# Kernel optimization log

Hardware: AMD Instinct MI355X
Metric: run time of the kernel (lower is better)

Reference implementation:

```python
import jax, jax.numpy as jnp
import numpy as np
import math

L = 2          # num_layers
H = 1024       # hidden_dim
NH = 16        # num_heads
HD = H // NH   # head_dim = 64
M = 4096       # mlp_dim
GRIDS = [(2, 32, 32), (1, 32, 32)]  # (t,h,w) per image -> 2048 + 1024 = 3072 tokens
THETA = 10000.0
EPS = 1e-5


def _rope_cos_sin(grids, head_dim):
    # Rope2DPosEmbRepeated: interleaved (x,y) complex rotations, repeated over t.
    n = head_dim // 4
    freqs = 1.0 / (THETA ** (np.arange(0, head_dim, 4, dtype=np.float64)[:n] / head_dim))
    parts = []
    for t, h, w in grids:
        ys, xs = np.meshgrid(np.arange(h), np.arange(w), indexing='ij')
        xa = xs.reshape(-1, 1).astype(np.float64) * freqs  # [h*w, n]
        ya = ys.reshape(-1, 1).astype(np.float64) * freqs
        ang = np.stack([xa, ya], axis=-1).reshape(-1, head_dim // 2)  # interleave x,y
        parts.append(np.tile(ang, (t, 1)))
    ang = np.concatenate(parts, axis=0).astype(np.float32)  # [S, head_dim//2]
    return jnp.asarray(np.cos(ang)), jnp.asarray(np.sin(ang))


def _segment_ids(grids):
    lens = [t * h * w for t, h, w in grids]
    return jnp.asarray(np.repeat(np.arange(len(lens)), lens))


def _layernorm(x, g, b):
    mu = jnp.mean(x, axis=-1, keepdims=True)
    var = jnp.mean(jnp.square(x - mu), axis=-1, keepdims=True)
    return (x - mu) * jax.lax.rsqrt(var + EPS) * g + b


def _apply_rope(x, cos, sin):
    # x: [S, NH, HD]; cos/sin: [S, HD//2] -> broadcast over heads (unsqueeze(-2))
    xr = x.reshape(x.shape[0], x.shape[1], HD // 2, 2)
    a, b = xr[..., 0], xr[..., 1]
    c = cos[:, None, :]
    s = sin[:, None, :]
    oa = a * c - b * s
    ob = a * s + b * c
    return jnp.stack([oa, ob], axis=-1).reshape(x.shape)


def setup_inputs() -> dict:
    key = jax.random.key(0)
    ks = jax.random.split(key, 8)
    S = sum(t * h * w for t, h, w in GRIDS)
    sH = 1.0 / math.sqrt(H)
    sM = 1.0 / math.sqrt(M)
    return {
        'hidden_states': jax.random.normal(ks[0], (S, H), jnp.float32),
        'grid_thws': jnp.asarray(np.array(GRIDS, dtype=np.int32)),
        'ln0_g': jnp.ones((L, H), jnp.float32),
        'ln0_b': jnp.zeros((L, H), jnp.float32),
        'wqkv': jax.random.normal(ks[1], (L, 3 * H, H), jnp.float32) * sH,
        'wo': jax.random.normal(ks[2], (L, H, H), jnp.float32) * sH,
        'ln1_g': jnp.ones((L, H), jnp.float32),
        'ln1_b': jnp.zeros((L, H), jnp.float32),
        'fc0_w': jax.random.normal(ks[3], (L, M, H), jnp.float32) * math.sqrt(2.0 / H),
        'fc0_b': jnp.zeros((L, M), jnp.float32),
        'fc1_w': jax.random.normal(ks[4], (L, H, M), jnp.float32) * math.sqrt(2.0 / M),
        'fc1_b': jnp.zeros((L, H), jnp.float32),
        'fln_g': jnp.ones((H,), jnp.float32),
        'fln_b': jnp.zeros((H,), jnp.float32),
    }


def reference(hidden_states, grid_thws, ln0_g, ln0_b, wqkv, wo, ln1_g, ln1_b,
              fc0_w, fc0_b, fc1_w, fc1_b, fln_g, fln_b):
    grids = [tuple(int(v) for v in row) for row in np.asarray(grid_thws)]
    S = hidden_states.shape[0]
    cos, sin = _rope_cos_sin(grids, HD)
    seg = _segment_ids(grids)
    mask = seg[:, None] == seg[None, :]  # block-diagonal [S, S]
    scale = 1.0 / math.sqrt(HD)

    x = hidden_states
    for i in range(L):
        h = _layernorm(x, ln0_g[i], ln0_b[i])
        qkv = (h @ wqkv[i].T).reshape(S, 3, NH, HD)
        q, k, v = qkv[:, 0], qkv[:, 1], qkv[:, 2]
        q = _apply_rope(q, cos, sin)
        k = _apply_rope(k, cos, sin)
        scores = jnp.einsum('qhd,khd->hqk', q, k) * scale
        scores = jnp.where(mask[None], scores, -1e30)
        attn = jax.nn.softmax(scores, axis=-1)
        o = jnp.einsum('hqk,khd->qhd', attn, v).reshape(S, H)
        x = x + o @ wo[i].T
        h2 = _layernorm(x, ln1_g[i], ln1_b[i])
        mlp = jax.nn.gelu(h2 @ fc0_w[i].T + fc0_b[i], approximate=False) @ fc1_w[i].T + fc1_b[i]
        x = x + mlp
    return _layernorm(x, fln_g, fln_b)
```

## Files before the change

kernel.cpp:

```cpp
#include <hip/hip_runtime.h>
#include <hip/hip_bf16.h>
#include <cstdint>
#include <math.h>

constexpr int ST   = 3072;
constexpr int HH   = 1024;
constexpr int NHD  = 16;
constexpr int DH   = 64;
constexpr int MMLP = 4096;
constexpr int SEG0 = 2048;

using short8 = __attribute__((ext_vector_type(8))) short;
using f32x4  = __attribute__((ext_vector_type(4))) float;

#if __has_builtin(__builtin_amdgcn_exp2f)
#define EXP2F __builtin_amdgcn_exp2f
#else
#define EXP2F exp2f
#endif

#if __has_builtin(__builtin_amdgcn_rcpf)
#define RCPF __builtin_amdgcn_rcpf
#else
#define RCPF(x) (1.f / (x))
#endif

__device__ __forceinline__ unsigned short f2bf(float f) {
  unsigned int u = __float_as_uint(f);
  u += 0x7fffu + ((u >> 16) & 1u);
  return (unsigned short)(u >> 16);
}

__device__ __forceinline__ float bf2f_lo(unsigned int u) {
  return __uint_as_float(u << 16);
}
__device__ __forceinline__ float bf2f_hi(unsigned int u) {
  return __uint_as_float(u & 0xffff0000u);
}

__device__ __forceinline__ void g2l16(const void* g, void* l) {
  __builtin_amdgcn_global_load_lds(
      (const __attribute__((address_space(1))) unsigned int*)g,
      (__attribute__((address_space(3))) unsigned int*)l, 16, 0, 0);
}

__device__ __forceinline__ float erf_fast(float z) {
  const float az = fabsf(z);
  const float t1 = RCPF(1.f + 0.3275911f * az);
  const float poly =
      t1 * (0.254829592f +
            t1 * (-0.284496736f +
                  t1 * (1.421413741f +
                        t1 * (-1.453152027f + t1 * 1.061405429f))));
  const float e = EXP2F(-az * az * 1.4426950408889634f);
  const float v = 1.f - poly * e;
  return (z < 0.f) ? -v : v;
}

__global__ void cast_all(const float* __restrict__ s0,
                         const float* __restrict__ s1,
                         const float* __restrict__ s2,
                         const float* __restrict__ s3,
                         ushort4* __restrict__ dst) {
  const int i = blockIdx.x * blockDim.x + threadIdx.x;
  const float4* src;
  int off;
  if (i < 1572864)      { src = (const float4*)s0; off = i; }
  else if (i < 2097152) { src = (const float4*)s1; off = i - 1572864; }
  else if (i < 4194304) { src = (const float4*)s2; off = i - 2097152; }
  else                  { src = (const float4*)s3; off = i - 4194304; }
  const float4 v = src[off];
  ushort4 u;
  u.x = f2bf(v.x); u.y = f2bf(v.y); u.z = f2bf(v.z); u.w = f2bf(v.w);
  dst[i] = u;
}

__global__ void ln_kernel(const float* __restrict__ x,
                          const float* __restrict__ g,
                          const float* __restrict__ b,
                          unsigned short* obf) {
  const int s = blockIdx.x;
  const int t = threadIdx.x;
  const float4 v = ((const float4*)(x + (size_t)s * HH))[t];
  float s1 = v.x + v.y + v.z + v.w;
  float s2 = v.x * v.x + v.y * v.y + v.z * v.z + v.w * v.w;
#pragma unroll
  for (int off = 32; off > 0; off >>= 1) {
    s1 += __shfl_down(s1, off);
    s2 += __shfl_down(s2, off);
  }
  __shared__ float red[8];
  __shared__ float stat[2];
  const int wv = t >> 6, ln = t & 63;
  if (ln == 0) { red[wv] = s1; red[4 + wv] = s2; }
  __syncthreads();
  if (t == 0) {
    float a1 = red[0] + red[1] + red[2] + red[3];
    float a2 = red[4] + red[5] + red[6] + red[7];
    float mu = a1 * (1.f / HH);
    float var = a2 * (1.f / HH) - mu * mu;
    stat[0] = mu;
    stat[1] = rsqrtf(var + 1e-5f);
  }
  __syncthreads();
  const float mu = stat[0], rs = stat[1];
  const float4 gg = ((const float4*)g)[t];
  const float4 bb = ((const float4*)b)[t];
  ushort4 u;
  u.x = f2bf((v.x - mu) * rs * gg.x + bb.x);
  u.y = f2bf((v.y - mu) * rs * gg.y + bb.y);
  u.z = f2bf((v.z - mu) * rs * gg.z + bb.z);
  u.w = f2bf((v.w - mu) * rs * gg.w + bb.w);
  ((ushort4*)(obf + (size_t)s * HH))[t] = u;
}

template <int NS>
__global__ void ln_comb(const float* __restrict__ xin,
                        const unsigned short* __restrict__ Pb,
                        const float* __restrict__ bias,
                        const float* __restrict__ g,
                        const float* __restrict__ b,
                        float* __restrict__ xout,
                        unsigned short* obf, float* of) {
  const int s = blockIdx.x;
  const int t = threadIdx.x;
  const size_t row = (size_t)s * HH;
  const size_t sl = (size_t)ST * HH;
  float4 v = ((const float4*)(xin + row))[t];
#pragma unroll
  for (int c = 0; c < NS; ++c) {
    const uint2 p = ((const uint2*)(Pb + c * sl + row))[t];
    v.x += bf2f_lo(p.x); v.y += bf2f_hi(p.x);
    v.z += bf2f_lo(p.y); v.w += bf2f_hi(p.y);
  }
  if (bias) {
    const float4 bb4 = ((const float4*)bias)[t];
    v.x += bb4.x; v.y += bb4.y; v.z += bb4.z; v.w += bb4.w;
  }
  if (xout) ((float4*)(xout + row))[t] = v;
  float s1 = v.x + v.y + v.z + v.w;
  float s2 = v.x * v.x + v.y * v.y + v.z * v.z + v.w * v.w;
#pragma unroll
  for (int off = 32; off > 0; off >>= 1) {
    s1 += __shfl_down(s1, off);
    s2 += __shfl_down(s2, off);
  }
  __shared__ float red[8];
  __shared__ float stat[2];
  const int wv = t >> 6, ln = t & 63;
  if (ln == 0) { red[wv] = s1; red[4 + wv] = s2; }
  __syncthreads();
  if (t == 0) {
    float a1 = red[0] + red[1] + red[2] + red[3];
    float a2 = red[4] + red[5] + red[6] + red[7];
    float mu = a1 * (1.f / HH);
    float var = a2 * (1.f / HH) - mu * mu;
    stat[0] = mu;
    stat[1] = rsqrtf(var + 1e-5f);
  }
  __syncthreads();
  const float mu = stat[0], rs = stat[1];
  const float4 gg = ((const float4*)g)[t];
  const float4 bb = ((const float4*)b)[t];
  float4 o;
  o.x = (v.x - mu) * rs * gg.x + bb.x;
  o.y = (v.y - mu) * rs * gg.y + bb.y;
  o.z = (v.z - mu) * rs * gg.z + bb.z;
  o.w = (v.w - mu) * rs * gg.w + bb.w;
  if (obf) {
    ushort4 u;
    u.x = f2bf(o.x); u.y = f2bf(o.y); u.z = f2bf(o.z); u.w = f2bf(o.w);
    ((ushort4*)(obf + row))[t] = u;
  } else {
    ((float4*)(of + row))[t] = o;
  }
}

__global__ void rope_tables(float2* __restrict__ cs2) {
  const int s = blockIdx.x;
  const int j = threadIdx.x;
  const int p = (s < SEG0) ? (s & 1023) : (s - SEG0);
  const int pos = (j & 1) ? (p >> 5) : (p & 31);
  const int f = j >> 1;
  const double freq = pow(10000.0, -(double)f / 16.0);
  const double ang = (double)pos * freq;
  cs2[s * 32 + j] = make_float2((float)cos(ang), (float)sin(ang));
}

template <int MODE>
__launch_bounds__(256)
__global__ void gemm_bt(const unsigned short* __restrict__ A,
                        const unsigned short* __restrict__ B,
                        float* Cf, unsigned short* Cb,
                        const float* __restrict__ bias,
                        int N, int K) {
  __shared__ unsigned short Sl[16384];
  unsigned short* Al = Sl;
  unsigned short* Bl = Sl + 8192;
  const int tid = threadIdx.x;
  const int lane = tid & 63;
  const int wave = tid >> 6;
  const int col = lane & 15;
  const int quad = lane >> 4;
  const int m0 = blockIdx.y * 128;
  const int n0 = blockIdx.x * 128;
  const int wm = (wave & 1) * 64;
  const int wn = (wave >> 1) * 64;

  int kFrom = 0, kTo = K;
  if (MODE == 4) {
    const int kc = K / gridDim.z;
    kFrom = blockIdx.z * kc;
    kTo = kFrom + kc;
  }

  f32x4 acc[4][4] = {};

  const int tr = tid >> 3;
  const int pb = tid & 7;
  const int kb = pb ^ (tr & 7);
  const unsigned short* Ag = A + (size_t)(m0 + tr) * K + kb * 8;
  const unsigned short* Bg = B + (size_t)(n0 + tr) * K + kb * 8;
  unsigned short* Alw = Al + (size_t)tid * 8;
  unsigned short* Blw = Bl + (size_t)tid * 8;

  for (int k0 = kFrom; k0 < kTo; k0 += 64) {
#pragma unroll
    for (int it = 0; it < 4; ++it) {
      g2l16(Ag + (size_t)(it * 32) * K + k0, Alw + it * 2048);
      g2l16(Bg + (size_t)(it * 32) * K + k0, Blw + it * 2048);
    }
    __syncthreads();
#pragma unroll
    for (int kk = 0; kk < 2; ++kk) {
      short8 af[4], bfr[4];
#pragma unroll
      for (int mt = 0; mt < 4; ++mt) {
        int r = wm + mt * 16 + col;
        int kp = (kk * 4 + quad) ^ (r & 7);
        af[mt] = *(const short8*)(Al + r * 64 + kp * 8);
      }
#pragma unroll
      for (int nt = 0; nt < 4; ++nt) {
        int r = wn + nt * 16 + col;
        int kp = (kk * 4 + quad) ^ (r & 7);
        bfr[nt] = *(const short8*)(Bl + r * 64 + kp * 8);
      }
#pragma unroll
      for (int mt = 0; mt < 4; ++mt)
#pragma unroll
        for (int nt = 0; nt < 4; ++nt)
          acc[mt][nt] = __builtin_amdgcn_mfma_f32_16x16x32_bf16(
              af[mt], bfr[nt], acc[mt][nt], 0, 0, 0);
    }
    __syncthreads();
  }

  if (MODE == 5) {
    const int bufsel = n0 >> 10;
    if (bufsel == 2) {
      unsigned int* T32 = (unsigned int*)Sl;
#pragma unroll
      for (int mt = 0; mt < 4; ++mt) {
        const int d0 = (wm + mt * 16 + quad * 4) >> 1;
#pragma unroll
        for (int nt = 0; nt < 4; ++nt) {
          const int cl = wn + nt * 16 + col;
          const int swz = (cl & 7) << 3;
          uint2 w;
          w.x = (unsigned)f2bf(acc[mt][nt][0]) |
                ((unsigned)f2bf(acc[mt][nt][1]) << 16);
          w.y = (unsigned)f2bf(acc[mt][nt][2]) |
                ((unsigned)f2bf(acc[mt][nt][3]) << 16);
          *(uint2*)&T32[cl * 64 + (d0 ^ swz)] = w;
        }
      }
      __syncthreads();
      unsigned short* vt = (unsigned short*)Cf;
      const int cl = tid >> 1;
      const int half = tid & 1;
      const int swz = (cl & 7) << 3;
      const int gch = (n0 & 1023) + cl;
      unsigned short* dst = vt + (size_t)gch * ST + m0 + half * 64;
#pragma unroll
      for (int j4 = 0; j4 < 8; ++j4) {
        const int d = half * 32 + j4 * 4;
        const uint4 v4 = *(const uint4*)&T32[cl * 64 + (d ^ swz)];
        *(uint4*)(dst + j4 * 8) = v4;
      }
    } else {
      const float2* tab = (const float2*)bias;
      unsigned short* out = Cb + (size_t)bufsel * (ST * HH);
      const float SQ = 0.125f * 1.4426950408889634f;
#pragma unroll
      for (int mt = 0; mt < 4; ++mt) {
#pragma unroll
        for (int r = 0; r < 4; ++r) {
          const int gr = m0 + wm + mt * 16 + quad * 4 + r;
#pragma unroll
          for (int nt = 0; nt < 4; ++nt) {
            const int gc = n0 + wn + nt * 16 + col;
            const int c1023 = gc & 1023;
            const int j = (c1023 & 63) >> 1;
            const float2 cs = tab[gr * 32 + j];
            const float v = acc[mt][nt][r];
            const float vp = __shfl_xor(v, 1);
            float res = (lane & 1) ? (vp * cs.y + v * cs.x)
                                   : (v * cs.x - vp * cs.y);
            if (bufsel == 0) res *= SQ;
            const float rp = __shfl_xor(res, 1);
            if (!(lane & 1))
              *(unsigned int*)(out + (size_t)gr * HH + c1023) =
                  (unsigned)f2bf(res) | ((unsigned)f2bf(rp) << 16);
          }
        }
      }
    }
    return;
  }
  const size_t zoff = (MODE == 4) ? (size_t)blockIdx.z * ST * N : 0;
#pragma unroll
  for (int mt = 0; mt < 4; ++mt) {
#pragma unroll
    for (int r = 0; r < 4; ++r) {
      const int gr = m0 + wm + mt * 16 + quad * 4 + r;
#pragma unroll
      for (int nt = 0; nt < 4; ++nt) {
        const int gc = n0 + wn + nt * 16 + col;
        const float v = acc[mt][nt][r];
        if (MODE == 2) {
          const float tt = v + bias[gc];
          const float gl = 0.5f * tt * (1.f + erf_fast(tt * 0.70710678f));
          Cb[(size_t)gr * N + gc] = f2bf(gl);
        } else {
          Cb[zoff + (size_t)gr * N + gc] = f2bf(v);
        }
      }
    }
  }
}

__launch_bounds__(256)
__global__ void attn_flash(const unsigned short* __restrict__ Qb,
                           const unsigned short* __restrict__ Kb,
                           const unsigned short* __restrict__ VT,
                           float* __restrict__ Op,
                           float* __restrict__ lbuf) {
  const int h = blockIdx.y;
  const int unit = blockIdx.x;
  int qt, chunk, s0;
  if (unit < 32) { qt = unit >> 1; chunk = unit & 1; s0 = 0; }
  else { qt = 16 + (unit - 32); chunk = 0; s0 = SEG0; }
  const int q0 = qt * 128;
  const int koff = s0 + chunk * 1024;

  const int tid = threadIdx.x;
  const int lane = tid & 63;
  const int wave = tid >> 6;
  const int col = lane & 15;
  const int quad = lane >> 4;

  __shared__ unsigned short Kl[128 * 64];
  __shared__ unsigned short Vl[64 * 128];
  __shared__ unsigned int Pl[4][2][2][16][20];

  short8 qf[2][2];
#pragma unroll
  for (int mt = 0; mt < 2; ++mt) {
    const unsigned short* qrow =
        Qb + (size_t)(q0 + wave * 32 + mt * 16 + col) * HH + h * DH;
    qf[mt][0] = *(const short8*)(qrow + quad * 8);
    qf[mt][1] = *(const short8*)(qrow + 32 + quad * 8);
  }

  short8 ones;
#pragma unroll
  for (int j = 0; j < 8; ++j) ones[j] = (short)0x3F80;

  f32x4 accO[2][4] = {};
  f32x4 accL[2] = {};
  const float SHIFT = 16.f;

  const int trK = tid >> 3, pbK = tid & 7;
  const int kbK = pbK ^ (trK & 7);
  const int trV = tid >> 4, pbV = tid & 15;

  for (int kb0 = 0; kb0 < 1024; kb0 += 128) {
#pragma unroll
    for (int it = 0; it < 4; ++it)
      g2l16(Kb + (size_t)(koff + kb0 + it * 32 + trK) * HH + h * DH + kbK * 8,
            (unsigned short*)Kl + it * 2048 + (size_t)tid * 8);
#pragma unroll
    for (int it = 0; it < 4; ++it) {
      const int d = it * 16 + trV;
      const int kbv = pbV ^ (d & 7);
      g2l16(VT + (size_t)(h * 64 + d) * ST + koff + kb0 + kbv * 8,
            (unsigned short*)Vl + it * 2048 + (size_t)tid * 8);
    }
    __syncthreads();

    f32x4 sc[2][8];
#pragma unroll
    for (int nt = 0; nt < 8; ++nt) {
      const int r = nt * 16 + col;
      const short8 kf0 = *(const short8*)(Kl + r * 64 + ((quad) ^ (r & 7)) * 8);
      const short8 kf1 = *(const short8*)(Kl + r * 64 + ((4 + quad) ^ (r & 7)) * 8);
#pragma unroll
      for (int mt = 0; mt < 2; ++mt) {
        f32x4 z = {};
        z = __builtin_amdgcn_mfma_f32_16x16x32_bf16(kf0, qf[mt][0], z, 0, 0, 0);
        sc[mt][nt] = __builtin_amdgcn_mfma_f32_16x16x32_bf16(kf1, qf[mt][1], z, 0, 0, 0);
      }
    }

#pragma unroll
    for (int kd = 0; kd < 4; ++kd) {
      const int par = kd & 1;
#pragma unroll
      for (int mt = 0; mt < 2; ++mt) {
#pragma unroll
        for (int ntl = 0; ntl < 2; ++ntl) {
          const f32x4 s4 = sc[mt][kd * 2 + ntl];
          const float p0 = EXP2F(s4[0] - SHIFT);
          const float p1 = EXP2F(s4[1] - SHIFT);
          const float p2 = EXP2F(s4[2] - SHIFT);
          const float p3 = EXP2F(s4[3] - SHIFT);
          uint2 w;
          w.x = (unsigned)f2bf(p0) | ((unsigned)f2bf(p1) << 16);
          w.y = (unsigned)f2bf(p2) | ((unsigned)f2bf(p3) << 16);
          *(uint2*)&Pl[wave][par][mt][col][ntl * 8 + quad * 2] = w;
        }
      }
      short8 pf[2];
#pragma unroll
      for (int mt = 0; mt < 2; ++mt)
        pf[mt] = *(const short8*)&Pl[wave][par][mt][col][quad * 4];
#pragma unroll
      for (int mt = 0; mt < 2; ++mt)
        accL[mt] = __builtin_amdgcn_mfma_f32_16x16x32_bf16(pf[mt], ones,
                                                           accL[mt], 0, 0, 0);
#pragma unroll
      for (int dt = 0; dt < 4; ++dt) {
        const int rv = dt * 16 + col;
        const int pbv2 = (kd * 4 + quad) ^ (rv & 7);
        const short8 vf = *(const short8*)(Vl + rv * 128 + pbv2 * 8);
#pragma unroll
        for (int mt = 0; mt < 2; ++mt)
          accO[mt][dt] = __builtin_amdgcn_mfma_f32_16x16x32_bf16(
              pf[mt], vf, accO[mt][dt], 0, 0, 0);
      }
    }
    __syncthreads();
  }

  float* Opc = Op + (size_t)chunk * (ST * HH);
#pragma unroll
  for (int mt = 0; mt < 2; ++mt)
#pragma unroll
    for (int r = 0; r < 4; ++r) {
      const int row = q0 + wave * 32 + mt * 16 + quad * 4 + r;
#pragma unroll
      for (int dt = 0; dt < 4; ++dt)
        Opc[(size_t)row * HH + h * DH + dt * 16 + col] = accO[mt][dt][r];
      if (col == 0)
        lbuf[((size_t)chunk * ST + row) * NHD + h] = accL[mt][r];
    }
}

__global__ void attn_combine(const float* __restrict__ Op,
                             const float* __restrict__ lbuf,
                             unsigned short* __restrict__ out) {
  const int s = blockIdx.x;
  const int t = threadIdx.x;
  const int h = t >> 4;
  const int d0 = (t & 15) * 4;
  const int nc = (s < SEG0) ? 2 : 1;
  float L = 0.f;
  float4 o = make_float4(0.f, 0.f, 0.f, 0.f);
  for (int c = 0; c < nc; ++c) {
    L += lbuf[((size_t)c * ST + s) * NHD + h];
    const float4 v =
        *(const float4*)(Op + (size_t)c * (ST * HH) + (size_t)s * HH + h * DH + d0);
    o.x += v.x; o.y += v.y; o.z += v.z; o.w += v.w;
  }
  const float inv = 1.f / L;
  ushort4 u;
  u.x = f2bf(o.x * inv); u.y = f2bf(o.y * inv);
  u.z = f2bf(o.z * inv); u.w = f2bf(o.w * inv);
  ((ushort4*)(out + (size_t)s * HH))[t] = u;
}

extern "C" void kernel_launch(void* const* d_in, const int* in_sizes, int n_in,
                              void* d_out, int out_size, void* d_ws, size_t ws_size,
                              hipStream_t stream) {
  const float* hs   = (const float*)d_in[0];
  const float* ln0g = (const float*)d_in[2];
  const float* ln0b = (const float*)d_in[3];
  const float* wqkv = (const float*)d_in[4];
  const float* wo   = (const float*)d_in[5];
  const float* ln1g = (const float*)d_in[6];
  const float* ln1b = (const float*)d_in[7];
  const float* fc0w = (const float*)d_in[8];
  const float* fc0b = (const float*)d_in[9];
  const float* fc1w = (const float*)d_in[10];
  const float* fc1b = (const float*)d_in[11];
  const float* fln_g = (const float*)d_in[12];
  const float* fln_b = (const float*)d_in[13];

  char* ws = (char*)d_ws;
  unsigned short* wqkv_bf = (unsigned short*)(ws + 0);
  unsigned short* wo_bf   = (unsigned short*)(ws + 12582912);
  unsigned short* fc0_bf  = (unsigned short*)(ws + 16777216);
  unsigned short* fc1_bf  = (unsigned short*)(ws + 33554432);
  float*          x       = (float*)(ws + 50331648);
  unsigned short* abf     = (unsigned short*)(ws + 62914560);
  unsigned short* gelu_bf = (unsigned short*)(ws + 69206016);
  unsigned short* Qbf     = (unsigned short*)(ws + 132120576);
  unsigned short* Kbf     = (unsigned short*)(ws + 138412032);
  float*          cs2tab  = (float*)(ws + 150994944);
  unsigned short* VT    = (unsigned short*)(ws + 94371840);
  float*          Op    = (float*)(ws + 100663296);
  float*          lbuf  = (float*)(ws + 144703488);
  unsigned short* Pbuf  = (unsigned short*)(ws + 94371840);

  cast_all<<<24576, 256, 0, stream>>>(wqkv, wo, fc0w, fc1w, (ushort4*)ws);
  rope_tables<<<ST, 32, 0, stream>>>((float2*)cs2tab);

  for (int i = 0; i < 2; ++i) {
    if (i == 0)
      ln_kernel<<<ST, 256, 0, stream>>>(hs, ln0g, ln0b, abf);
    gemm_bt<5><<<dim3(24, 24), 256, 0, stream>>>(
        abf, wqkv_bf + (size_t)i * 3 * HH * HH, (float*)VT, Qbf, cs2tab,
        3 * HH, HH);
    attn_flash<<<dim3(40, 16), 256, 0, stream>>>(Qbf, Kbf, VT, Op, lbuf);
    attn_combine<<<ST, 256, 0, stream>>>(Op, lbuf, abf);
    gemm_bt<4><<<dim3(8, 24, 2), 256, 0, stream>>>(
        abf, wo_bf + (size_t)i * HH * HH, nullptr, Pbuf, nullptr, HH, HH);
    ln_comb<2><<<ST, 256, 0, stream>>>(
        (i == 0) ? hs : x, Pbuf, nullptr, ln1g + i * HH, ln1b + i * HH,
        x, abf, nullptr);
    gemm_bt<2><<<dim3(32, 24), 256, 0, stream>>>(
        abf, fc0_bf + (size_t)i * MMLP * HH, nullptr, gelu_bf, fc0b + i * MMLP,
        MMLP, HH);
    gemm_bt<4><<<dim3(8, 24, 2), 256, 0, stream>>>(
        gelu_bf, fc1_bf + (size_t)i * HH * MMLP, nullptr, Pbuf, nullptr,
        HH, MMLP);
    if (i == 0)
      ln_comb<2><<<ST, 256, 0, stream>>>(x, Pbuf, fc1b, ln0g + HH, ln0b + HH,
                                         x, abf, nullptr);
    else
      ln_comb<2><<<ST, 256, 0, stream>>>(x, Pbuf, fc1b + HH, fln_g, fln_b,
                                         nullptr, nullptr, (float*)d_out);
  }
}
```

Measured before the change: 606.7 us.

## Split attention keys into more chunks and alias P buffer onto K/V LDS

Doubles the number of key chunks per query tile in the flash attention kernel (4 chunks of 512 keys for the first segment, 2 for the second), launching twice as many blocks so more of the GPU is occupied. The P staging buffer now reuses the K tile's shared memory after an extra barrier, cutting LDS per block so up to 5 blocks can fit per CU (launch bounds raised). The combine kernel sums more partial outputs, and the extra partials are stored in the GELU buffer region, which adds memory traffic for the partial outputs and the combine step.

After: 799.2 us. 1.32x slower.

```diff
diff --git a/kernel.cpp b/kernel.cpp
--- a/kernel.cpp
+++ b/kernel.cpp
@@ -340,19 +340,20 @@
   }
 }
 
-__launch_bounds__(256)
+__launch_bounds__(256, 5)
 __global__ void attn_flash(const unsigned short* __restrict__ Qb,
                            const unsigned short* __restrict__ Kb,
                            const unsigned short* __restrict__ VT,
-                           float* __restrict__ Op,
+                           float* __restrict__ Op01,
+                           float* __restrict__ Op23,
                            float* __restrict__ lbuf) {
   const int h = blockIdx.y;
   const int unit = blockIdx.x;
   int qt, chunk, s0;
-  if (unit < 32) { qt = unit >> 1; chunk = unit & 1; s0 = 0; }
-  else { qt = 16 + (unit - 32); chunk = 0; s0 = SEG0; }
+  if (unit < 64) { qt = unit >> 2; chunk = unit & 3; s0 = 0; }
+  else { const int u = unit - 64; qt = 16 + (u >> 1); chunk = u & 1; s0 = SEG0; }
   const int q0 = qt * 128;
-  const int koff = s0 + chunk * 1024;
+  const int koff = s0 + chunk * 512;
 
   const int tid = threadIdx.x;
   const int lane = tid & 63;
@@ -360,9 +361,10 @@
   const int col = lane & 15;
   const int quad = lane >> 4;
 
-  __shared__ unsigned short Kl[128 * 64];
-  __shared__ unsigned short Vl[64 * 128];
-  __shared__ unsigned int Pl[4][2][2][16][20];
+  __shared__ unsigned short Sl[16384];
+  unsigned short* Kl = Sl;
+  unsigned short* Vl = Sl + 8192;
+  unsigned int* Plb = (unsigned int*)Sl;
 
   short8 qf[2][2];
 #pragma unroll
@@ -384,8 +386,9 @@
   const int trK = tid >> 3, pbK = tid & 7;
   const int kbK = pbK ^ (trK & 7);
   const int trV = tid >> 4, pbV = tid & 15;
-
-  for (int kb0 = 0; kb0 < 1024; kb0 += 128) {
+  const int prow = ((wave * 2) * 16 + col) * 20;
+
+  for (int kb0 = 0; kb0 < 512; kb0 += 128) {
 #pragma unroll
     for (int it = 0; it < 4; ++it)
       g2l16(Kb + (size_t)(koff + kb0 + it * 32 + trK) * HH + h * DH + kbK * 8,
@@ -412,10 +415,10 @@
         sc[mt][nt] = __builtin_amdgcn_mfma_f32_16x16x32_bf16(kf1, qf[mt][1], z, 0, 0, 0);
       }
     }
+    __syncthreads();
 
 #pragma unroll
     for (int kd = 0; kd < 4; ++kd) {
-      const int par = kd & 1;
 #pragma unroll
       for (int mt = 0; mt < 2; ++mt) {
 #pragma unroll
@@ -428,13 +431,13 @@
           uint2 w;
           w.x = (unsigned)f2bf(p0) | ((unsigned)f2bf(p1) << 16);
           w.y = (unsigned)f2bf(p2) | ((unsigned)f2bf(p3) << 16);
-          *(uint2*)&Pl[wave][par][mt][col][ntl * 8 + quad * 2] = w;
+          *(uint2*)&Plb[prow + mt * 320 + ntl * 8 + quad * 2] = w;
         }
       }
       short8 pf[2];
 #pragma unroll
       for (int mt = 0; mt < 2; ++mt)
-        pf[mt] = *(const short8*)&Pl[wave][par][mt][col][quad * 4];
+        pf[mt] = *(const short8*)&Plb[prow + mt * 320 + quad * 4];
 #pragma unroll
       for (int mt = 0; mt < 2; ++mt)
         accL[mt] = __builtin_amdgcn_mfma_f32_16x16x32_bf16(pf[mt], ones,
@@ -453,7 +456,8 @@
     __syncthreads();
   }
 
-  float* Opc = Op + (size_t)chunk * (ST * HH);
+  float* Opc = (chunk < 2) ? (Op01 + (size_t)chunk * (ST * HH))
+                           : (Op23 + (size_t)(chunk - 2) * (ST * HH));
 #pragma unroll
   for (int mt = 0; mt < 2; ++mt)
 #pragma unroll
@@ -467,20 +471,22 @@
     }
 }
 
-__global__ void attn_combine(const float* __restrict__ Op,
+__global__ void attn_combine(const float* __restrict__ Op01,
+                             const float* __restrict__ Op23,
                              const float* __restrict__ lbuf,
                              unsigned short* __restrict__ out) {
   const int s = blockIdx.x;
   const int t = threadIdx.x;
   const int h = t >> 4;
   const int d0 = (t & 15) * 4;
-  const int nc = (s < SEG0) ? 2 : 1;
+  const int nc = (s < SEG0) ? 4 : 2;
   float L = 0.f;
   float4 o = make_float4(0.f, 0.f, 0.f, 0.f);
   for (int c = 0; c < nc; ++c) {
+    const float* Opc = (c < 2) ? (Op01 + (size_t)c * (ST * HH))
+                               : (Op23 + (size_t)(c - 2) * (ST * HH));
     L += lbuf[((size_t)c * ST + s) * NHD + h];
-    const float4 v =
-        *(const float4*)(Op + (size_t)c * (ST * HH) + (size_t)s * HH + h * DH + d0);
+    const float4 v = *(const float4*)(Opc + (size_t)s * HH + h * DH + d0);
     o.x += v.x; o.y += v.y; o.z += v.z; o.w += v.w;
   }
   const float inv = 1.f / L;
@@ -520,6 +526,7 @@
   float*          cs2tab  = (float*)(ws + 150994944);
   unsigned short* VT    = (unsigned short*)(ws + 94371840);
   float*          Op    = (float*)(ws + 100663296);
+  float*          Op23  = (float*)(ws + 69206016);
   float*          lbuf  = (float*)(ws + 144703488);
   unsigned short* Pbuf  = (unsigned short*)(ws + 94371840);
 
@@ -532,8 +539,8 @@
     gemm_bt<5><<<dim3(24, 24), 256, 0, stream>>>(
         abf, wqkv_bf + (size_t)i * 3 * HH * HH, (float*)VT, Qbf, cs2tab,
         3 * HH, HH);
-    attn_flash<<<dim3(40, 16), 256, 0, stream>>>(Qbf, Kbf, VT, Op, lbuf);
-    attn_combine<<<ST, 256, 0, stream>>>(Op, lbuf, abf);
+    attn_flash<<<dim3(80, 16), 256, 0, stream>>>(Qbf, Kbf, VT, Op, Op23, lbuf);
+    attn_combine<<<ST, 256, 0, stream>>>(Op, Op23, lbuf, abf);
     gemm_bt<4><<<dim3(8, 24, 2), 256, 0, stream>>>(
         abf, wo_bf + (size_t)i * HH * HH, nullptr, Pbuf, nullptr, HH, HH);
     ln_comb<2><<<ST, 256, 0, stream>>>(
```
